# Optimization experiments

Hardware: AMD Instinct MI355X
Metric: run time of the kernel (lower is better)

Reference implementation:

```python
import jax, jax.numpy as jnp
import numpy as np

N_NODES = 50000
N_EDGES = 800000
IN_CH = 64
HID = 128
LAST_HID = 256


def setup_inputs() -> dict:
    key = jax.random.key(0)
    ks = jax.random.split(key, 12)
    x = jax.random.normal(ks[0], (N_NODES, IN_CH), dtype=jnp.float32)
    edge_index = jax.random.randint(ks[1], (2, N_EDGES), 0, N_NODES, dtype=jnp.int64)
    s = lambda fan_in: 1.0 / np.sqrt(fan_in)
    return {
        "x": x,
        "edge_index": edge_index,
        # SAGEConv1: lin_l (aggregated neighbors, with bias), lin_r (root, no bias)
        "W1l": jax.random.normal(ks[2], (HID, IN_CH), dtype=jnp.float32) * s(IN_CH),
        "b1l": jnp.zeros((HID,), dtype=jnp.float32),
        "W1r": jax.random.normal(ks[3], (HID, IN_CH), dtype=jnp.float32) * s(IN_CH),
        # SAGEConv2 -> 1 channel
        "W2l": jax.random.normal(ks[4], (1, HID), dtype=jnp.float32) * s(HID),
        "b2l": jnp.zeros((1,), dtype=jnp.float32),
        "W2r": jax.random.normal(ks[5], (1, HID), dtype=jnp.float32) * s(HID),
        # fc1 (LazyLinear bound to N_NODES input features) and fc2
        "fc1_W": jax.random.normal(ks[6], (LAST_HID, N_NODES), dtype=jnp.float32) * s(N_NODES),
        "fc1_b": jnp.zeros((LAST_HID,), dtype=jnp.float32),
        "fc2_W": jax.random.normal(ks[7], (1, LAST_HID), dtype=jnp.float32) * s(LAST_HID),
        "fc2_b": jnp.zeros((1,), dtype=jnp.float32),
    }


def _sage_conv(h, src, dst, Wl, bl, Wr, n_nodes):
    # PyG SAGEConv (mean aggr): out = lin_l(mean_{j in N(i)} x_j) + lin_r(x_i)
    msgs = h[src]  # [E, F] gather of source node features
    summed = jax.ops.segment_sum(msgs, dst, num_segments=n_nodes)  # [N, F]
    deg = jax.ops.segment_sum(jnp.ones((src.shape[0],), h.dtype), dst, num_segments=n_nodes)
    agg = summed / jnp.maximum(deg, 1.0)[:, None]
    return agg @ Wl.T + bl + h @ Wr.T


def reference(x, edge_index, W1l, b1l, W1r, W2l, b2l, W2r, fc1_W, fc1_b, fc2_W, fc2_b):
    n = x.shape[0]
    src, dst = edge_index[0], edge_index[1]
    h = jax.nn.relu(_sage_conv(x, src, dst, W1l, b1l, W1r, n))   # [N, HID]
    h = jax.nn.relu(_sage_conv(h, src, dst, W2l, b2l, W2r, n))   # [N, 1]
    v = h[:, 0]                                                   # [N]
    z = fc1_W @ v + fc1_b                                         # [LAST_HID]
    pred = fc2_W @ z + fc2_b                                      # [1]
    return pred[0]  # scalar (torch.squeeze)
```

## Files before the change

### kernel.cpp

```cpp
#include <hip/hip_runtime.h>

#define N_NODESC 50000
#define N_EDGESC 800000
#define MAXDEG 64

typedef short bf16x8 __attribute__((ext_vector_type(8)));
typedef short short4v __attribute__((ext_vector_type(4)));
typedef float f32x4  __attribute__((ext_vector_type(4)));

__device__ inline unsigned short f2bf(float f) {
    unsigned u = __float_as_uint(f);
    unsigned r = u + 0x7FFFu + ((u >> 16) & 1u);
    return (unsigned short)(r >> 16);
}
__device__ inline float bf2f(unsigned short h) {
    return __uint_as_float(((unsigned)h) << 16);
}

__global__ void kW0_init_pack(const float* __restrict__ W1l, const float* __restrict__ W1r,
                              short* __restrict__ pkhi, short* __restrict__ pklo,
                              int* __restrict__ deg, float* __restrict__ z) {
    int i = blockIdx.x * 256 + threadIdx.x;
    if (i < N_NODESC) deg[i] = 0;
    if (i < 256) z[i] = 0.0f;
    if (blockIdx.x < 4) {
        int ks = blockIdx.x;
        int t  = threadIdx.x;
        int o  = t & 127;
        int h  = t >> 7;
        const float* src = (ks < 2) ? (W1r + o * 64 + ks * 32)
                                    : (W1l + o * 64 + (ks - 2) * 32);
        #pragma unroll
        for (int qi = 0; qi < 2; qi++) {
            int q = 2 * h + qi;
            float4 a = *(const float4*)(src + q * 8);
            float4 b = *(const float4*)(src + q * 8 + 4);
            float v[8] = {a.x, a.y, a.z, a.w, b.x, b.y, b.z, b.w};
            bf16x8 hv, lv;
            #pragma unroll
            for (int j = 0; j < 8; j++) {
                unsigned short hh = f2bf(v[j]);
                hv[j] = (short)hh;
                lv[j] = (short)f2bf(v[j] - bf2f(hh));
            }
            int idx = ((ks * 4 + q) * 128 + o) * 8;
            *(bf16x8*)&pkhi[idx] = hv;
            *(bf16x8*)&pklo[idx] = lv;
        }
    }
}

#define K1_BLOCKS 2048
#define K1_EPB 1563
__global__ void k1_bucket(const int* __restrict__ ei, int* __restrict__ deg,
                          int* __restrict__ bucket) {
    int g   = blockIdx.x & 3;
    int idx = blockIdx.x >> 2;
    int lo = g * (N_NODESC / 4), hi = lo + (N_NODESC / 4);
    int e0 = idx * K1_EPB;
    for (int i = threadIdx.x; i < K1_EPB; i += 256) {
        int e = e0 + i;
        if (e < N_EDGESC) {
            int dst = ei[N_EDGESC + e];
            int src = ei[e];
            if (dst >= lo && dst < hi) {
                int slot = atomicAdd(&deg[dst], 1);
                if (slot < MAXDEG) bucket[dst * MAXDEG + slot] = src;
            }
        }
    }
}

#define K3S 144
#define K3BLK 32

__launch_bounds__(256, 3)
__global__ void k3_fused(const float* __restrict__ x,
                         const int* __restrict__ deg, const int* __restrict__ bucket,
                         const short* __restrict__ pkhi, const short* __restrict__ pklo,
                         const float* __restrict__ b1l,
                         const float* __restrict__ W2l, const float* __restrict__ W2r,
                         float* __restrict__ s_out, float* __restrict__ t_out) {
    __shared__ __align__(16) short sAhi[K3BLK * K3S];
    __shared__ __align__(16) short sAlo[K3BLK * K3S];
    __shared__ float sSp[4][K3BLK], sTp[4][K3BLK];

    int tid = threadIdx.x;
    int lane = tid & 63;
    int wave = tid >> 6;
    int col = lane & 15;
    int quad = lane >> 4;
    int node0 = blockIdx.x * K3BLK;

    float4 sv0, sv1;
    {
        int n = tid >> 3, kc = tid & 7;
        int node = node0 + n;
        if (node < N_NODESC) {
            const float* src = x + node * 64 + kc * 8;
            sv0 = *(const float4*)src;
            sv1 = *(const float4*)(src + 4);
        } else {
            sv0 = make_float4(0.f, 0.f, 0.f, 0.f);
            sv1 = make_float4(0.f, 0.f, 0.f, 0.f);
        }
    }

    {
        int n = tid >> 3, kc = tid & 7;
        float v[8] = {sv0.x, sv0.y, sv0.z, sv0.w, sv1.x, sv1.y, sv1.z, sv1.w};
        bf16x8 hv, lv;
        #pragma unroll
        for (int j = 0; j < 8; j++) {
            unsigned short h = f2bf(v[j]);
            hv[j] = (short)h;
            lv[j] = (short)f2bf(v[j] - bf2f(h));
        }
        *(bf16x8*)&sAhi[n * K3S + kc * 8] = hv;
        *(bf16x8*)&sAlo[n * K3S + kc * 8] = lv;
    }

    {
        int base = node0 + wave * 8;
        int dA = 0, bA = 0, dB = 0, bB = 0;
        if (base < N_NODESC)     { dA = deg[base];     bA = bucket[base * MAXDEG + lane]; }
        if (base + 1 < N_NODESC) { dB = deg[base + 1]; bB = bucket[(base + 1) * MAXDEG + lane]; }
        for (int np = 0; np < 4; np++) {
            int nN = base + 2 * np + 2;
            int dA2 = 0, bA2 = 0, dB2 = 0, bB2 = 0;
            if (np < 3) {
                if (nN < N_NODESC)     { dA2 = deg[nN];     bA2 = bucket[nN * MAXDEG + lane]; }
                if (nN + 1 < N_NODESC) { dB2 = deg[nN + 1]; bB2 = bucket[(nN + 1) * MAXDEG + lane]; }
            }
            int cA = min(dA, MAXDEG);
            int cB = min(dB, MAXDEG);
            int kmax = max(cA, cB);
            float4 aA = make_float4(0.f, 0.f, 0.f, 0.f);
            float4 aB = make_float4(0.f, 0.f, 0.f, 0.f);
            for (int k = 0; k < kmax; k += 8) {
                int i0 = k + quad, i1 = k + 4 + quad;
                int a0 = __shfl(bA, i0);
                int a1 = __shfl(bA, i1);
                int b0 = __shfl(bB, i0);
                int b1 = __shfl(bB, i1);
                if (i0 < cA) {
                    float4 v = ((const float4*)(x + a0 * 64))[col];
                    aA.x += v.x; aA.y += v.y; aA.z += v.z; aA.w += v.w;
                }
                if (i1 < cA) {
                    float4 v = ((const float4*)(x + a1 * 64))[col];
                    aA.x += v.x; aA.y += v.y; aA.z += v.z; aA.w += v.w;
                }
                if (i0 < cB) {
                    float4 v = ((const float4*)(x + b0 * 64))[col];
                    aB.x += v.x; aB.y += v.y; aB.z += v.z; aB.w += v.w;
                }
                if (i1 < cB) {
                    float4 v = ((const float4*)(x + b1 * 64))[col];
                    aB.x += v.x; aB.y += v.y; aB.z += v.z; aB.w += v.w;
                }
            }
            #pragma unroll
            for (int m = 16; m <= 32; m <<= 1) {
                aA.x += __shfl_xor(aA.x, m);
                aA.y += __shfl_xor(aA.y, m);
                aA.z += __shfl_xor(aA.z, m);
                aA.w += __shfl_xor(aA.w, m);
                aB.x += __shfl_xor(aB.x, m);
                aB.y += __shfl_xor(aB.y, m);
                aB.z += __shfl_xor(aB.z, m);
                aB.w += __shfl_xor(aB.w, m);
            }
            if (quad == 0) {
                int nlocA = wave * 8 + 2 * np;
                float invA = 1.0f / (float)max(dA, 1);
                float invB = 1.0f / (float)max(dB, 1);
                float vA[4] = {aA.x * invA, aA.y * invA, aA.z * invA, aA.w * invA};
                float vB[4] = {aB.x * invB, aB.y * invB, aB.z * invB, aB.w * invB};
                short4v hvA, lvA, hvB, lvB;
                #pragma unroll
                for (int j = 0; j < 4; j++) {
                    unsigned short hA = f2bf(vA[j]);
                    hvA[j] = (short)hA;
                    lvA[j] = (short)f2bf(vA[j] - bf2f(hA));
                    unsigned short hB = f2bf(vB[j]);
                    hvB[j] = (short)hB;
                    lvB[j] = (short)f2bf(vB[j] - bf2f(hB));
                }
                *(short4v*)&sAhi[nlocA * K3S + 64 + col * 4] = hvA;
                *(short4v*)&sAlo[nlocA * K3S + 64 + col * 4] = lvA;
                *(short4v*)&sAhi[(nlocA + 1) * K3S + 64 + col * 4] = hvB;
                *(short4v*)&sAlo[(nlocA + 1) * K3S + 64 + col * 4] = lvB;
            }
            dA = dA2; bA = bA2; dB = dB2; bB = bB2;
        }
    }

    int o_base = wave * 32;
    bf16x8 bhi[2][4], blo[2][4];
    float bias_r[2], w2l_r[2], w2r_r[2];
    #pragma unroll
    for (int oc = 0; oc < 2; oc++) {
        int o = o_base + oc * 16 + col;
        bias_r[oc] = b1l[o]; w2l_r[oc] = W2l[o]; w2r_r[oc] = W2r[o];
        #pragma unroll
        for (int ks = 0; ks < 4; ks++) {
            int idx = ((ks * 4 + quad) * 128 + o) * 8;
            bhi[oc][ks] = *(const bf16x8*)&pkhi[idx];
            blo[oc][ks] = *(const bf16x8*)&pklo[idx];
        }
    }
    __syncthreads();

    f32x4 acc[2][2];
    #pragma unroll
    for (int nt = 0; nt < 2; nt++)
        #pragma unroll
        for (int oc = 0; oc < 2; oc++) acc[nt][oc] = (f32x4)0.f;

    #pragma unroll
    for (int ks = 0; ks < 4; ks++) {
        #pragma unroll
        for (int nt = 0; nt < 2; nt++) {
            int off = (nt * 16 + col) * K3S + ks * 32 + quad * 8;
            bf16x8 ah = *(const bf16x8*)&sAhi[off];
            bf16x8 al = *(const bf16x8*)&sAlo[off];
            #pragma unroll
            for (int oc = 0; oc < 2; oc++) {
                acc[nt][oc] = __builtin_amdgcn_mfma_f32_16x16x32_bf16(ah, bhi[oc][ks], acc[nt][oc], 0, 0, 0);
                acc[nt][oc] = __builtin_amdgcn_mfma_f32_16x16x32_bf16(al, bhi[oc][ks], acc[nt][oc], 0, 0, 0);
                acc[nt][oc] = __builtin_amdgcn_mfma_f32_16x16x32_bf16(ah, blo[oc][ks], acc[nt][oc], 0, 0, 0);
            }
        }
    }

    #pragma unroll
    for (int nt = 0; nt < 2; nt++) {
        float sp[4] = {0.f, 0.f, 0.f, 0.f};
        float tp[4] = {0.f, 0.f, 0.f, 0.f};
        #pragma unroll
        for (int oc = 0; oc < 2; oc++)
            #pragma unroll
            for (int reg = 0; reg < 4; reg++) {
                float h = fmaxf(acc[nt][oc][reg] + bias_r[oc], 0.f);
                sp[reg] += h * w2l_r[oc];
                tp[reg] += h * w2r_r[oc];
            }
        #pragma unroll
        for (int reg = 0; reg < 4; reg++) {
            #pragma unroll
            for (int m = 1; m <= 8; m <<= 1) {
                sp[reg] += __shfl_xor(sp[reg], m);
                tp[reg] += __shfl_xor(tp[reg], m);
            }
        }
        if (col == 0) {
            int nn = nt * 16 + quad * 4;
            #pragma unroll
            for (int reg = 0; reg < 4; reg++) {
                sSp[wave][nn + reg] = sp[reg];
                sTp[wave][nn + reg] = tp[reg];
            }
        }
    }
    __syncthreads();
    if (tid < K3BLK) {
        int node = node0 + tid;
        if (node < N_NODESC) {
            s_out[node] = sSp[0][tid] + sSp[1][tid] + sSp[2][tid] + sSp[3][tid];
            t_out[node] = sTp[0][tid] + sTp[1][tid] + sTp[2][tid] + sTp[3][tid];
        }
    }
}

__global__ void k4_layer2(const float* __restrict__ s, const float* __restrict__ t,
                          const int* __restrict__ deg, const int* __restrict__ bucket,
                          const float* __restrict__ b2l, float* __restrict__ v) {
    int tid = threadIdx.x;
    int lane = tid & 15;
    int node = blockIdx.x * 16 + (tid >> 4);
    int d = deg[node];
    int c = min(d, MAXDEG);
    float sum = 0.f;
    for (int k = lane; k < c; k += 16) sum += s[bucket[node * MAXDEG + k]];
    sum += __shfl_xor(sum, 1);
    sum += __shfl_xor(sum, 2);
    sum += __shfl_xor(sum, 4);
    sum += __shfl_xor(sum, 8);
    if (lane == 0) {
        float h = sum / (float)max(d, 1) + b2l[0] + t[node];
        v[node] = fmaxf(h, 0.f);
    }
}

__global__ void k5_fc1(const float* __restrict__ fc1W, const float* __restrict__ v,
                       float* __restrict__ z) {
    int row = blockIdx.x >> 2;
    int part = blockIdx.x & 3;
    const float4* W4 = (const float4*)(fc1W + row * 50000 + part * 12500);
    const float4* v4 = (const float4*)(v + part * 12500);
    float sum = 0.f;
    for (int i = threadIdx.x; i < 3125; i += 256) {
        float4 w = W4[i], a = v4[i];
        sum += w.x * a.x + w.y * a.y + w.z * a.z + w.w * a.w;
    }
    #pragma unroll
    for (int m = 1; m < 64; m <<= 1) sum += __shfl_xor(sum, m);
    __shared__ float red[4];
    if ((threadIdx.x & 63) == 0) red[threadIdx.x >> 6] = sum;
    __syncthreads();
    if (threadIdx.x == 0) atomicAdd(&z[row], red[0] + red[1] + red[2] + red[3]);
}

__global__ void k6_head(const float* __restrict__ z, const float* __restrict__ fc1b,
                        const float* __restrict__ fc2W, const float* __restrict__ fc2b,
                        float* __restrict__ out) {
    int t = threadIdx.x;
    float val = (z[t] + fc1b[t]) * fc2W[t];
    #pragma unroll
    for (int m = 1; m < 64; m <<= 1) val += __shfl_xor(val, m);
    __shared__ float red[4];
    if ((t & 63) == 0) red[t >> 6] = val;
    __syncthreads();
    if (t == 0) out[0] = red[0] + red[1] + red[2] + red[3] + fc2b[0];
}

extern "C" void kernel_launch(void* const* d_in, const int* in_sizes, int n_in,
                              void* d_out, int out_size, void* d_ws, size_t ws_size,
                              hipStream_t stream) {
    const float* x    = (const float*)d_in[0];
    const int*   ei   = (const int*)d_in[1];
    const float* W1l  = (const float*)d_in[2];
    const float* b1l  = (const float*)d_in[3];
    const float* W1r  = (const float*)d_in[4];
    const float* W2l  = (const float*)d_in[5];
    const float* b2l  = (const float*)d_in[6];
    const float* W2r  = (const float*)d_in[7];
    const float* fc1W = (const float*)d_in[8];
    const float* fc1b = (const float*)d_in[9];
    const float* fc2W = (const float*)d_in[10];
    const float* fc2b = (const float*)d_in[11];
    float* out = (float*)d_out;

    char* ws = (char*)d_ws;
    int*   deg    = (int*)  (ws + 0);
    float* z      = (float*)(ws + 200192);
    int*   bucket = (int*)  (ws + 201216);
    float* s      = (float*)(ws + 13001216);
    float* t      = (float*)(ws + 13201216);
    float* v      = (float*)(ws + 13401216);
    short* pkhi   = (short*)(ws + 13601280);
    short* pklo   = (short*)(ws + 13634048);

    kW0_init_pack<<<196,  256, 0, stream>>>(W1l, W1r, pkhi, pklo, deg, z);
    k1_bucket    <<<K1_BLOCKS, 256, 0, stream>>>(ei, deg, bucket);
    k3_fused     <<<1563, 256, 0, stream>>>(x, deg, bucket, pkhi, pklo, b1l, W2l, W2r, s, t);
    k4_layer2    <<<3125, 256, 0, stream>>>(s, t, deg, bucket, b2l, v);
    k5_fc1       <<<1024, 256, 0, stream>>>(fc1W, v, z);
    k6_head      <<<1,    256, 0, stream>>>(z, fc1b, fc2W, fc2b, out);
}
```

Before: 207.5 us.

## Double k3_fused block to 512 threads, halving per-wave gather and MFMA work

The fused layer-1 kernel now runs 8 waves per block instead of 4. Each wave gathers neighbours for 4 nodes instead of 8 and computes 16 output channels instead of 32. The x staging is re-split so each thread loads one float4, and the layer-2 partial sums are reduced over 8 waves. The aim is more concurrent waves to hide the latency of the irregular neighbour gather, at the cost of a larger block, more LDS reduction and more synchronisation overhead per block.

```diff
diff --git a/kernel.cpp b/kernel.cpp
--- a/kernel.cpp
+++ b/kernel.cpp
@@ -74,7 +74,7 @@
 #define K3S 144
 #define K3BLK 32
 
-__launch_bounds__(256, 3)
+__launch_bounds__(512, 4)
 __global__ void k3_fused(const float* __restrict__ x,
                          const int* __restrict__ deg, const int* __restrict__ bucket,
                          const short* __restrict__ pkhi, const short* __restrict__ pklo,
@@ -83,7 +83,7 @@
                          float* __restrict__ s_out, float* __restrict__ t_out) {
     __shared__ __align__(16) short sAhi[K3BLK * K3S];
     __shared__ __align__(16) short sAlo[K3BLK * K3S];
-    __shared__ float sSp[4][K3BLK], sTp[4][K3BLK];
+    __shared__ float sSp[8][K3BLK], sTp[8][K3BLK];
 
     int tid = threadIdx.x;
     int lane = tid & 63;
@@ -92,43 +92,39 @@
     int quad = lane >> 4;
     int node0 = blockIdx.x * K3BLK;
 
-    float4 sv0, sv1;
+    float4 sv;
     {
-        int n = tid >> 3, kc = tid & 7;
+        int n = tid >> 4, kc = tid & 15;
         int node = node0 + n;
         if (node < N_NODESC) {
-            const float* src = x + node * 64 + kc * 8;
-            sv0 = *(const float4*)src;
-            sv1 = *(const float4*)(src + 4);
+            sv = *(const float4*)(x + node * 64 + kc * 4);
         } else {
-            sv0 = make_float4(0.f, 0.f, 0.f, 0.f);
-            sv1 = make_float4(0.f, 0.f, 0.f, 0.f);
-        }
-    }
-
+            sv = make_float4(0.f, 0.f, 0.f, 0.f);
+        }
+    }
     {
-        int n = tid >> 3, kc = tid & 7;
-        float v[8] = {sv0.x, sv0.y, sv0.z, sv0.w, sv1.x, sv1.y, sv1.z, sv1.w};
-        bf16x8 hv, lv;
-        #pragma unroll
-        for (int j = 0; j < 8; j++) {
+        int n = tid >> 4, kc = tid & 15;
+        float v[4] = {sv.x, sv.y, sv.z, sv.w};
+        short4v hv, lv;
+        #pragma unroll
+        for (int j = 0; j < 4; j++) {
             unsigned short h = f2bf(v[j]);
             hv[j] = (short)h;
             lv[j] = (short)f2bf(v[j] - bf2f(h));
         }
-        *(bf16x8*)&sAhi[n * K3S + kc * 8] = hv;
-        *(bf16x8*)&sAlo[n * K3S + kc * 8] = lv;
+        *(short4v*)&sAhi[n * K3S + kc * 4] = hv;
+        *(short4v*)&sAlo[n * K3S + kc * 4] = lv;
     }
 
     {
-        int base = node0 + wave * 8;
+        int base = node0 + wave * 4;
         int dA = 0, bA = 0, dB = 0, bB = 0;
         if (base < N_NODESC)     { dA = deg[base];     bA = bucket[base * MAXDEG + lane]; }
         if (base + 1 < N_NODESC) { dB = deg[base + 1]; bB = bucket[(base + 1) * MAXDEG + lane]; }
-        for (int np = 0; np < 4; np++) {
+        for (int np = 0; np < 2; np++) {
             int nN = base + 2 * np + 2;
             int dA2 = 0, bA2 = 0, dB2 = 0, bB2 = 0;
-            if (np < 3) {
+            if (np < 1) {
                 if (nN < N_NODESC)     { dA2 = deg[nN];     bA2 = bucket[nN * MAXDEG + lane]; }
                 if (nN + 1 < N_NODESC) { dB2 = deg[nN + 1]; bB2 = bucket[(nN + 1) * MAXDEG + lane]; }
             }
@@ -172,7 +168,7 @@
                 aB.w += __shfl_xor(aB.w, m);
             }
             if (quad == 0) {
-                int nlocA = wave * 8 + 2 * np;
+                int nlocA = wave * 4 + 2 * np;
                 float invA = 1.0f / (float)max(dA, 1);
                 float invB = 1.0f / (float)max(dB, 1);
                 float vA[4] = {aA.x * invA, aA.y * invA, aA.z * invA, aA.w * invA};
@@ -196,27 +192,20 @@
         }
     }
 
-    int o_base = wave * 32;
-    bf16x8 bhi[2][4], blo[2][4];
-    float bias_r[2], w2l_r[2], w2r_r[2];
-    #pragma unroll
-    for (int oc = 0; oc < 2; oc++) {
-        int o = o_base + oc * 16 + col;
-        bias_r[oc] = b1l[o]; w2l_r[oc] = W2l[o]; w2r_r[oc] = W2r[o];
-        #pragma unroll
-        for (int ks = 0; ks < 4; ks++) {
-            int idx = ((ks * 4 + quad) * 128 + o) * 8;
-            bhi[oc][ks] = *(const bf16x8*)&pkhi[idx];
-            blo[oc][ks] = *(const bf16x8*)&pklo[idx];
-        }
+    int o = wave * 16 + col;
+    bf16x8 bhi[4], blo[4];
+    float bias_r = b1l[o], w2l_r = W2l[o], w2r_r = W2r[o];
+    #pragma unroll
+    for (int ks = 0; ks < 4; ks++) {
+        int idx = ((ks * 4 + quad) * 128 + o) * 8;
+        bhi[ks] = *(const bf16x8*)&pkhi[idx];
+        blo[ks] = *(const bf16x8*)&pklo[idx];
     }
     __syncthreads();
 
-    f32x4 acc[2][2];
-    #pragma unroll
-    for (int nt = 0; nt < 2; nt++)
-        #pragma unroll
-        for (int oc = 0; oc < 2; oc++) acc[nt][oc] = (f32x4)0.f;
+    f32x4 acc[2];
+    acc[0] = (f32x4)0.f;
+    acc[1] = (f32x4)0.f;
 
     #pragma unroll
     for (int ks = 0; ks < 4; ks++) {
@@ -225,27 +214,21 @@
             int off = (nt * 16 + col) * K3S + ks * 32 + quad * 8;
             bf16x8 ah = *(const bf16x8*)&sAhi[off];
             bf16x8 al = *(const bf16x8*)&sAlo[off];
-            #pragma unroll
-            for (int oc = 0; oc < 2; oc++) {
-                acc[nt][oc] = __builtin_amdgcn_mfma_f32_16x16x32_bf16(ah, bhi[oc][ks], acc[nt][oc], 0, 0, 0);
-                acc[nt][oc] = __builtin_amdgcn_mfma_f32_16x16x32_bf16(al, bhi[oc][ks], acc[nt][oc], 0, 0, 0);
-                acc[nt][oc] = __builtin_amdgcn_mfma_f32_16x16x32_bf16(ah, blo[oc][ks], acc[nt][oc], 0, 0, 0);
-            }
+            acc[nt] = __builtin_amdgcn_mfma_f32_16x16x32_bf16(ah, bhi[ks], acc[nt], 0, 0, 0);
+            acc[nt] = __builtin_amdgcn_mfma_f32_16x16x32_bf16(al, bhi[ks], acc[nt], 0, 0, 0);
+            acc[nt] = __builtin_amdgcn_mfma_f32_16x16x32_bf16(ah, blo[ks], acc[nt], 0, 0, 0);
         }
     }
 
     #pragma unroll
     for (int nt = 0; nt < 2; nt++) {
-        float sp[4] = {0.f, 0.f, 0.f, 0.f};
-        float tp[4] = {0.f, 0.f, 0.f, 0.f};
-        #pragma unroll
-        for (int oc = 0; oc < 2; oc++)
-            #pragma unroll
-            for (int reg = 0; reg < 4; reg++) {
-                float h = fmaxf(acc[nt][oc][reg] + bias_r[oc], 0.f);
-                sp[reg] += h * w2l_r[oc];
-                tp[reg] += h * w2r_r[oc];
-            }
+        float sp[4], tp[4];
+        #pragma unroll
+        for (int reg = 0; reg < 4; reg++) {
+            float h = fmaxf(acc[nt][reg] + bias_r, 0.f);
+            sp[reg] = h * w2l_r;
+            tp[reg] = h * w2r_r;
+        }
         #pragma unroll
         for (int reg = 0; reg < 4; reg++) {
             #pragma unroll
@@ -267,8 +250,11 @@
     if (tid < K3BLK) {
         int node = node0 + tid;
         if (node < N_NODESC) {
-            s_out[node] = sSp[0][tid] + sSp[1][tid] + sSp[2][tid] + sSp[3][tid];
-            t_out[node] = sTp[0][tid] + sTp[1][tid] + sTp[2][tid] + sTp[3][tid];
+            float ssum = 0.f, tsum = 0.f;
+            #pragma unroll
+            for (int w = 0; w < 8; w++) { ssum += sSp[w][tid]; tsum += sTp[w][tid]; }
+            s_out[node] = ssum;
+            t_out[node] = tsum;
         }
     }
 }
@@ -354,7 +340,7 @@
 
     kW0_init_pack<<<196,  256, 0, stream>>>(W1l, W1r, pkhi, pklo, deg, z);
     k1_bucket    <<<K1_BLOCKS, 256, 0, stream>>>(ei, deg, bucket);
-    k3_fused     <<<1563, 256, 0, stream>>>(x, deg, bucket, pkhi, pklo, b1l, W2l, W2r, s, t);
+    k3_fused     <<<1563, 512, 0, stream>>>(x, deg, bucket, pkhi, pklo, b1l, W2l, W2r, s, t);
     k4_layer2    <<<3125, 256, 0, stream>>>(s, t, deg, bucket, b2l, v);
     k5_fc1       <<<1024, 256, 0, stream>>>(fc1W, v, z);
     k6_head      <<<1,    256, 0, stream>>>(z, fc1b, fc2W, fc2b, out);
```

Result: faster. 201.9 us (-2.7%).
